# Kernel optimization log

Hardware: AMD Instinct MI355X
Metric: run time of the kernel (lower is better)

The kernel has to match this reference:

```python
import jax, jax.numpy as jnp
import numpy as np

EPS = 1e-6  # LayerNorm eps (added to std, matching torch code)
H = 4       # n_heads
B, D, N, DFF = 8, 512, 1024, 1024


def layer_norm(x, g, b):
    # torch: a_2 * (x - mean) / (std + eps) + b_2, std unbiased (ddof=1)
    m = x.mean(-1, keepdims=True)
    s = x.std(-1, ddof=1, keepdims=True)
    return g * (x - m) / (s + EPS) + b


def mha(q, k, v, W, b):
    # W: [4, d, d] (in->out), b: [4, d]; heads H, d_k = d // H
    Bq, Nq, d = q.shape
    dk = d // H

    def proj(x, i):
        return (x @ W[i] + b[i]).reshape(Bq, -1, H, dk).transpose(0, 2, 1, 3)

    Q, K, V = proj(q, 0), proj(k, 1), proj(v, 2)
    scores = jnp.einsum('bhqd,bhkd->bhqk', Q, K) / np.sqrt(dk).astype(np.float32)
    p = jax.nn.softmax(scores, axis=-1)
    o = jnp.einsum('bhqk,bhkd->bhqd', p, V).transpose(0, 2, 1, 3).reshape(Bq, -1, d)
    return o @ W[3] + b[3]


def ffn(x, w1, b1, w2, b2):
    return jax.nn.relu(x @ w1 + b1) @ w2 + b2


def encoder(x, aw, ab, fw1, fb1, fw2, fb2, lg, lb):
    x = x + mha(layer_norm(x, lg[0], lb[0]), layer_norm(x, lg[0], lb[0]), layer_norm(x, lg[0], lb[0]), aw, ab)
    x = x + ffn(layer_norm(x, lg[1], lb[1]), fw1, fb1, fw2, fb2)
    return layer_norm(x, lg[2], lb[2])


def decoder(x, mem, sw, sb, cw, cb, fw1, fb1, fw2, fb2, lg, lb):
    h0 = layer_norm(x, lg[0], lb[0])
    x = x + mha(h0, h0, h0, sw, sb)
    h1 = layer_norm(x, lg[1], lb[1])
    x = x + mha(h1, mem, mem, cw, cb)
    x = x + ffn(layer_norm(x, lg[2], lb[2]), fw1, fb1, fw2, fb2)
    return layer_norm(x, lg[3], lb[3])


def model(src, tgt, p):
    # src, tgt: [B, N, D]
    mem = encoder(src, p['enc_attn_w'], p['enc_attn_b'], p['enc_ff_w1'], p['enc_ff_b1'],
                  p['enc_ff_w2'], p['enc_ff_b2'], p['enc_ln_g'], p['enc_ln_b'])
    return decoder(tgt, mem, p['dec_sa_w'], p['dec_sa_b'], p['dec_ca_w'], p['dec_ca_b'],
                   p['dec_ff_w1'], p['dec_ff_b1'], p['dec_ff_w2'], p['dec_ff_b2'],
                   p['dec_ln_g'], p['dec_ln_b'])


def setup_inputs() -> dict:
    key = jax.random.key(0)
    ks = jax.random.split(key, 12)
    sc = 0.02
    return {
        'src': jax.random.normal(ks[0], (B, D, N), jnp.float32),
        'tgt': jax.random.normal(ks[1], (B, D, N), jnp.float32),
        'enc_attn_w': jax.random.normal(ks[2], (4, D, D), jnp.float32) * sc,
        'enc_attn_b': jnp.zeros((4, D), jnp.float32),
        'enc_ff_w1': jax.random.normal(ks[3], (D, DFF), jnp.float32) * sc,
        'enc_ff_b1': jnp.zeros((DFF,), jnp.float32),
        'enc_ff_w2': jax.random.normal(ks[4], (DFF, D), jnp.float32) * sc,
        'enc_ff_b2': jnp.zeros((D,), jnp.float32),
        'enc_ln_g': jnp.ones((3, D), jnp.float32),
        'enc_ln_b': jnp.zeros((3, D), jnp.float32),
        'dec_sa_w': jax.random.normal(ks[5], (4, D, D), jnp.float32) * sc,
        'dec_sa_b': jnp.zeros((4, D), jnp.float32),
        'dec_ca_w': jax.random.normal(ks[6], (4, D, D), jnp.float32) * sc,
        'dec_ca_b': jnp.zeros((4, D), jnp.float32),
        'dec_ff_w1': jax.random.normal(ks[7], (D, DFF), jnp.float32) * sc,
        'dec_ff_b1': jnp.zeros((DFF,), jnp.float32),
        'dec_ff_w2': jax.random.normal(ks[8], (DFF, D), jnp.float32) * sc,
        'dec_ff_b2': jnp.zeros((D,), jnp.float32),
        'dec_ln_g': jnp.ones((4, D), jnp.float32),
        'dec_ln_b': jnp.zeros((4, D), jnp.float32),
    }


def reference(src, tgt, enc_attn_w, enc_attn_b, enc_ff_w1, enc_ff_b1, enc_ff_w2, enc_ff_b2,
              enc_ln_g, enc_ln_b, dec_sa_w, dec_sa_b, dec_ca_w, dec_ca_b,
              dec_ff_w1, dec_ff_b1, dec_ff_w2, dec_ff_b2, dec_ln_g, dec_ln_b):
    p = dict(enc_attn_w=enc_attn_w, enc_attn_b=enc_attn_b, enc_ff_w1=enc_ff_w1,
             enc_ff_b1=enc_ff_b1, enc_ff_w2=enc_ff_w2, enc_ff_b2=enc_ff_b2,
             enc_ln_g=enc_ln_g, enc_ln_b=enc_ln_b, dec_sa_w=dec_sa_w, dec_sa_b=dec_sa_b,
             dec_ca_w=dec_ca_w, dec_ca_b=dec_ca_b, dec_ff_w1=dec_ff_w1, dec_ff_b1=dec_ff_b1,
             dec_ff_w2=dec_ff_w2, dec_ff_b2=dec_ff_b2, dec_ln_g=dec_ln_g, dec_ln_b=dec_ln_b)
    s = src.transpose(0, 2, 1)  # [B, N, D]
    t = tgt.transpose(0, 2, 1)
    tgt_embedding = model(s, t, p).transpose(0, 2, 1)  # [B, D, N]
    src_embedding = model(t, s, p).transpose(0, 2, 1)
    return (src_embedding, tgt_embedding)
```

## Files before the change

### kernel.cpp

```cpp
#include <hip/hip_runtime.h>

#define BB 8
#define NN 1024
#define DD 512
#define DFFK 1024
#define HH 4
#define RR (BB * NN)
#define MM (2 * RR)

typedef unsigned short u16;
typedef u16 u16x8 __attribute__((ext_vector_type(8)));
typedef u16 u16x4 __attribute__((ext_vector_type(4)));
typedef float f32x4 __attribute__((ext_vector_type(4)));
typedef __bf16 bf16x8 __attribute__((ext_vector_type(8)));

__device__ __forceinline__ u16 f32_to_bf16(float f) {
  unsigned int u = __builtin_bit_cast(unsigned int, f);
  unsigned int r = u + 0x7FFFu + ((u >> 16) & 1u);
  return (u16)(r >> 16);
}

__device__ __forceinline__ f32x4 mfma16(u16x8 a, u16x8 b, f32x4 c) {
  return __builtin_amdgcn_mfma_f32_16x16x32_bf16(
      __builtin_bit_cast(bf16x8, a), __builtin_bit_cast(bf16x8, b), c, 0, 0, 0);
}

__device__ __forceinline__ void gl16(u16* lds, const u16* g) {
  __builtin_amdgcn_global_load_lds(
      (const __attribute__((address_space(1))) unsigned int*)g,
      (__attribute__((address_space(3))) unsigned int*)lds, 16, 0, 0);
}

__global__ __launch_bounds__(256) void wconv_kernel(const float* __restrict__ W,
                                                    u16* __restrict__ Wt, int K, int N2, int nmat) {
  int idx = blockIdx.x * 256 + threadIdx.x;
  if (idx >= nmat * K * N2) return;
  int mat = idx / (K * N2), rem = idx % (K * N2);
  int k = rem % K, n = rem / K;
  Wt[(size_t)mat * K * N2 + (size_t)n * K + k] =
      f32_to_bf16(W[(size_t)mat * K * N2 + (size_t)k * N2 + n]);
}

__global__ __launch_bounds__(256) void transpose_kernel(const float* __restrict__ in,
                                                        float* __restrict__ out, int R_, int C_) {
  __shared__ float t[32][33];
  int bx = blockIdx.x * 32, by = blockIdx.y * 32;
  size_t zoff = (size_t)blockIdx.z * R_ * C_;
  const float* ip = in + zoff;
  float* op = out + zoff;
  int tx = threadIdx.x, ty = threadIdx.y;
#pragma unroll
  for (int i = 0; i < 32; i += 8)
    t[ty + i][tx] = ip[(size_t)(by + ty + i) * C_ + bx + tx];
  __syncthreads();
#pragma unroll
  for (int i = 0; i < 32; i += 8)
    op[(size_t)(bx + ty + i) * R_ + by + tx] = t[tx][ty + i];
}

__global__ __launch_bounds__(256) void out_trans_kernel(const float* __restrict__ in,
                                                        float* __restrict__ outA,
                                                        float* __restrict__ outB) {
  __shared__ float t[32][33];
  int z = blockIdx.z;
  int dx = blockIdx.x * 32;
  int sy = blockIdx.y * 32;
  int tx = threadIdx.x, ty = threadIdx.y;
  const float* ip = in + (size_t)z * NN * DD;
#pragma unroll
  for (int i = 0; i < 32; i += 8)
    t[ty + i][tx] = ip[(size_t)(sy + ty + i) * DD + dx + tx];
  __syncthreads();
  float* dst = (z < BB) ? (outA + (size_t)z * DD * NN) : (outB + (size_t)(z - BB) * DD * NN);
#pragma unroll
  for (int i = 0; i < 32; i += 8)
    dst[(size_t)(dx + ty + i) * NN + sy + tx] = t[tx][ty + i];
}

__global__ __launch_bounds__(256) void vtrans_kernel(const u16* __restrict__ V, int vstride,
                                                     u16* __restrict__ Vt) {
  __shared__ u16 t[32][33];
  int z = blockIdx.z;
  int b = z >> 2, h = z & 3;
  int sx = blockIdx.x * 32;
  int dy = blockIdx.y * 32;
  int tx = threadIdx.x, ty = threadIdx.y;
  const u16* ip = V + (size_t)b * NN * vstride + h * 128 + dy;
#pragma unroll
  for (int i = 0; i < 32; i += 8)
    t[ty + i][tx] = ip[(size_t)(sx + ty + i) * vstride + tx];
  __syncthreads();
  u16* op = Vt + ((size_t)z * 128 + dy) * NN + sx;
#pragma unroll
  for (int i = 0; i < 32; i += 8)
    op[(size_t)(ty + i) * NN + tx] = t[tx][ty + i];
}

template <int OUTBF>
__global__ __launch_bounds__(256) void ln_kernel(const float* __restrict__ x0,
                                                 const float* __restrict__ x1,
                                                 const float* __restrict__ g,
                                                 const float* __restrict__ bb,
                                                 void* __restrict__ out) {
  int l = threadIdx.x & 63, w = threadIdx.x >> 6;
  size_t row = (size_t)blockIdx.x * 4 + w;
  const float* xr = (row < RR) ? (x0 + row * DD) : (x1 + (row - RR) * DD);
  float4 v0 = *(const float4*)(xr + l * 8);
  float4 v1 = *(const float4*)(xr + l * 8 + 4);
  float sum = v0.x + v0.y + v0.z + v0.w + v1.x + v1.y + v1.z + v1.w;
  float sq = v0.x * v0.x + v0.y * v0.y + v0.z * v0.z + v0.w * v0.w +
             v1.x * v1.x + v1.y * v1.y + v1.z * v1.z + v1.w * v1.w;
#pragma unroll
  for (int o = 1; o < 64; o <<= 1) {
    sum += __shfl_xor(sum, o);
    sq += __shfl_xor(sq, o);
  }
  float mean = sum * (1.0f / DD);
  float var = fmaxf((sq - (float)DD * mean * mean) * (1.0f / (DD - 1)), 0.0f);
  float inv = 1.0f / (sqrtf(var) + 1e-6f);
  float4 g0 = *(const float4*)(g + l * 8), g1 = *(const float4*)(g + l * 8 + 4);
  float4 b0 = *(const float4*)(bb + l * 8), b1 = *(const float4*)(bb + l * 8 + 4);
  float xs[8] = {v0.x, v0.y, v0.z, v0.w, v1.x, v1.y, v1.z, v1.w};
  float gs[8] = {g0.x, g0.y, g0.z, g0.w, g1.x, g1.y, g1.z, g1.w};
  float bs[8] = {b0.x, b0.y, b0.z, b0.w, b1.x, b1.y, b1.z, b1.w};
  float y[8];
#pragma unroll
  for (int j = 0; j < 8; j++) y[j] = (xs[j] - mean) * inv * gs[j] + bs[j];
  if (OUTBF) {
    u16x8 o8;
#pragma unroll
    for (int j = 0; j < 8; j++) o8[j] = f32_to_bf16(y[j]);
    *(u16x8*)((u16*)out + row * DD + l * 8) = o8;
  } else {
    float4 o0 = {y[0], y[1], y[2], y[3]};
    float4 o1 = {y[4], y[5], y[6], y[7]};
    *(float4*)((float*)out + row * DD + l * 8) = o0;
    *(float4*)((float*)out + row * DD + l * 8 + 4) = o1;
  }
}

template <bool RELU, bool OUT_BF16, bool HAS_RES>
__global__ __launch_bounds__(256, 3) void gemm_bt(const u16* __restrict__ A, int lda,
                                                  const u16* __restrict__ Bt,
                                                  const float* __restrict__ bias,
                                                  const float* res0, const float* res1,
                                                  void* Cout, int ldc,
                                                  int N2, int Kd) {
  __shared__ u16 sA[3][512 * 8];
  __shared__ u16 sB[3][512 * 8];
  int tid = threadIdx.x;
  int l = tid & 63, w = tid >> 6;
  int wm = (w >> 1) * 64, wn = (w & 1) * 64;
  int m0 = blockIdx.x * 128, n0 = blockIdx.y * 128;
  f32x4 acc[4][4] = {};

  auto stage = [&](int buf, int k0) {
#pragma unroll
    for (int is = 0; is < 2; is++) {
      int slot = is * 256 + w * 64 + l;
      int chunk = slot >> 7, row = slot & 127;
      gl16(&sA[buf][(size_t)(is * 256 + w * 64) * 8],
           A + (size_t)(m0 + row) * lda + k0 + chunk * 8);
      gl16(&sB[buf][(size_t)(is * 256 + w * 64) * 8],
           Bt + (size_t)(n0 + row) * Kd + k0 + chunk * 8);
    }
  };
  int nt = Kd >> 5;
  stage(0, 0);
  stage(1, 32);
  int bi = 0;
  for (int t = 0; t < nt; t++) {
    if (t + 1 < nt) asm volatile("s_waitcnt vmcnt(4)" ::: "memory");
    else            asm volatile("s_waitcnt vmcnt(0)" ::: "memory");
    __builtin_amdgcn_s_barrier();
    __builtin_amdgcn_sched_barrier(0);
    if (t + 2 < nt) {
      int b2 = bi + 2; if (b2 >= 3) b2 -= 3;
      stage(b2, (t + 2) * 32);
    }
    u16x8 af[4], bf[4];
#pragma unroll
    for (int i = 0; i < 4; i++) {
      af[i] = *(const u16x8*)&sA[bi][((l >> 4) * 128 + wm + i * 16 + (l & 15)) * 8];
      bf[i] = *(const u16x8*)&sB[bi][((l >> 4) * 128 + wn + i * 16 + (l & 15)) * 8];
    }
    __builtin_amdgcn_s_setprio(1);
#pragma unroll
    for (int i = 0; i < 4; i++)
#pragma unroll
      for (int j = 0; j < 4; j++) acc[i][j] = mfma16(af[i], bf[j], acc[i][j]);
    __builtin_amdgcn_s_setprio(0);
    bi = (bi == 2) ? 0 : bi + 1;
  }
  __syncthreads();
  float* eTw = (float*)&sA[0][0] + w * 1024;
  float4 bias4 = *(const float4*)&bias[n0 + wn + (l & 15) * 4];
#pragma unroll
  for (int i = 0; i < 4; i++) {
#pragma unroll
    for (int j = 0; j < 4; j++)
#pragma unroll
      for (int r = 0; r < 4; r++)
        eTw[((l >> 4) * 4 + r) * 64 + j * 16 + (l & 15)] = acc[i][j][r];
#pragma unroll
    for (int t = 0; t < 4; t++) {
      int row = t * 4 + (l >> 4);
      int f4 = l & 15;
      float4 v4 = *(float4*)&eTw[row * 64 + f4 * 4];
      int gm = m0 + wm + i * 16 + row;
      int gn = n0 + wn + f4 * 4;
      v4.x += bias4.x; v4.y += bias4.y; v4.z += bias4.z; v4.w += bias4.w;
      if (RELU) {
        v4.x = fmaxf(v4.x, 0.0f); v4.y = fmaxf(v4.y, 0.0f);
        v4.z = fmaxf(v4.z, 0.0f); v4.w = fmaxf(v4.w, 0.0f);
      }
      if (HAS_RES) {
        const float* rp = (gm < RR) ? (res0 + (size_t)gm * DD)
                                    : (res1 + (size_t)(gm - RR) * DD);
        float4 r4 = *(const float4*)&rp[gn];
        v4.x += r4.x; v4.y += r4.y; v4.z += r4.z; v4.w += r4.w;
      }
      if (OUT_BF16) {
        u16x4 o4;
        o4[0] = f32_to_bf16(v4.x); o4[1] = f32_to_bf16(v4.y);
        o4[2] = f32_to_bf16(v4.z); o4[3] = f32_to_bf16(v4.w);
        *(u16x4*)&((u16*)Cout)[(size_t)gm * ldc + gn] = o4;
      } else {
        *(float4*)&((float*)Cout)[(size_t)gm * ldc + gn] = v4;
      }
    }
  }
}

__global__ __launch_bounds__(512, 4) void attn_kernel(const u16* __restrict__ Q, int qstride,
                                                      const u16* __restrict__ K, int kstride,
                                                      const u16* __restrict__ Vt,
                                                      u16* __restrict__ O, int ostride) {
  __shared__ u16 sK[2][64 * 128];
  __shared__ u16 sV[2][128 * 64];
  __shared__ u16 sP[8][16 * 64];
  int tid = threadIdx.x;
  int l = tid & 63, w = tid >> 6;
  int p = blockIdx.x;
  int xcd = p & 7, slot = p >> 3;
  int qb = slot & 7, ghigh = slot >> 3;
  int g = ghigh * 8 + xcd;
  int b = g >> 2, h = g & 3;
  int q0 = qb * 128 + w * 16;
  int bh = g;

  const u16* Qg = Q + (size_t)b * NN * qstride + h * 128;
  const u16* Kg = K + (size_t)b * NN * kstride + h * 128;
  const u16* Vg = Vt + (size_t)bh * 128 * NN;

  u16x8 qf[4];
#pragma unroll
  for (int c = 0; c < 4; c++)
    qf[c] = *(const u16x8*)(Qg + (size_t)(q0 + (l & 15)) * qstride + c * 32 + (l >> 4) * 8);

  f32x4 oacc[8] = {};
  float psum[4] = {0.0f, 0.0f, 0.0f, 0.0f};
  const float scale = 0.08838834764831843f;

  auto stage = [&](int buf, int k0) {
#pragma unroll
    for (int is = 0; is < 2; is++) {
      int slot2 = is * 512 + tid;
      {
        int row = slot2 >> 4, c16 = slot2 & 15;
        int colb = (c16 * 16) ^ ((row & 7) << 4);
        gl16(&sK[buf][(size_t)(is * 512 + w * 64) * 8],
             Kg + (size_t)(k0 + row) * kstride + (colb >> 1));
      }
      {
        int drow = slot2 >> 3, c16 = slot2 & 7;
        int colb = (c16 * 16) ^ ((drow & 7) << 4);
        gl16(&sV[buf][(size_t)(is * 512 + w * 64) * 8],
             Vg + (size_t)drow * NN + k0 + (colb >> 1));
      }
    }
  };

  stage(0, 0);
  int buf = 0;
  for (int t = 0; t < NN / 64; t++) {
    __syncthreads();
    if (t + 1 < NN / 64) stage(buf ^ 1, (t + 1) * 64);
    f32x4 sc[4] = {};
    __builtin_amdgcn_s_setprio(1);
#pragma unroll
    for (int ks = 0; ks < 4; ks++) {
      int row = ks * 16 + (l & 15);
      int swz = (row & 7) << 4;
#pragma unroll
      for (int c = 0; c < 4; c++) {
        int colb = (c * 64 + (l >> 4) * 16) ^ swz;
        u16x8 kf = *(const u16x8*)&sK[buf][row * 128 + (colb >> 1)];
        sc[ks] = mfma16(qf[c], kf, sc[ks]);
      }
    }
    __builtin_amdgcn_s_setprio(0);
#pragma unroll
    for (int r = 0; r < 4; r++) {
      int prow = (l >> 4) * 4 + r;
      int pswz = (prow & 7) << 4;
#pragma unroll
      for (int ks = 0; ks < 4; ks++) {
        float pp = __expf(sc[ks][r] * scale);
        psum[r] += pp;
        int colb = ((ks * 16 + (l & 15)) * 2) ^ pswz;
        sP[w][prow * 64 + (colb >> 1)] = f32_to_bf16(pp);
      }
    }
    u16x8 pf[2];
#pragma unroll
    for (int kc = 0; kc < 2; kc++) {
      int prow = l & 15;
      int colb = (kc * 64 + (l >> 4) * 16) ^ ((prow & 7) << 4);
      pf[kc] = *(const u16x8*)&sP[w][prow * 64 + (colb >> 1)];
    }
    __builtin_amdgcn_s_setprio(1);
#pragma unroll
    for (int n = 0; n < 8; n++) {
      int drow = n * 16 + (l & 15);
      int swz = (drow & 7) << 4;
#pragma unroll
      for (int kc = 0; kc < 2; kc++) {
        int colb = (kc * 64 + (l >> 4) * 16) ^ swz;
        u16x8 vf = *(const u16x8*)&sV[buf][drow * 64 + (colb >> 1)];
        oacc[n] = mfma16(pf[kc], vf, oacc[n]);
      }
    }
    __builtin_amdgcn_s_setprio(0);
    buf ^= 1;
  }
#pragma unroll
  for (int r = 0; r < 4; r++) {
    psum[r] += __shfl_xor(psum[r], 1);
    psum[r] += __shfl_xor(psum[r], 2);
    psum[r] += __shfl_xor(psum[r], 4);
    psum[r] += __shfl_xor(psum[r], 8);
  }
#pragma unroll
  for (int r = 0; r < 4; r++) {
    float inv = 1.0f / psum[r];
    int grow = q0 + (l >> 4) * 4 + r;
    u16* Op = O + ((size_t)b * NN + grow) * ostride + h * 128 + (l & 15);
#pragma unroll
    for (int n = 0; n < 8; n++) Op[n * 16] = f32_to_bf16(oacc[n][r] * inv);
  }
}

extern "C" void kernel_launch(void* const* d_in, const int* in_sizes, int n_in,
                              void* d_out, int out_size, void* d_ws, size_t ws_size,
                              hipStream_t stream) {
  const float* src = (const float*)d_in[0];
  const float* tgt = (const float*)d_in[1];
  const float* enc_attn_w = (const float*)d_in[2];
  const float* enc_attn_b = (const float*)d_in[3];
  const float* enc_ff_w1 = (const float*)d_in[4];
  const float* enc_ff_b1 = (const float*)d_in[5];
  const float* enc_ff_w2 = (const float*)d_in[6];
  const float* enc_ff_b2 = (const float*)d_in[7];
  const float* enc_ln_g = (const float*)d_in[8];
  const float* enc_ln_b = (const float*)d_in[9];
  const float* dec_sa_w = (const float*)d_in[10];
  const float* dec_sa_b = (const float*)d_in[11];
  const float* dec_ca_w = (const float*)d_in[12];
  const float* dec_ca_b = (const float*)d_in[13];
  const float* dec_ff_w1 = (const float*)d_in[14];
  const float* dec_ff_b1 = (const float*)d_in[15];
  const float* dec_ff_w2 = (const float*)d_in[16];
  const float* dec_ff_b2 = (const float*)d_in[17];
  const float* dec_ln_g = (const float*)d_in[18];
  const float* dec_ln_b = (const float*)d_in[19];

  u16* wp = (u16*)d_ws;
  u16* wE = wp;   wp += 4 * DD * DD;
  u16* wS = wp;   wp += 4 * DD * DD;
  u16* wC = wp;   wp += 4 * DD * DD;
  u16* wEff1 = wp; wp += DD * DFFK;
  u16* wEff2 = wp; wp += DD * DFFK;
  u16* wDff1 = wp; wp += DD * DFFK;
  u16* wDff2 = wp; wp += DD * DFFK;
  char* p = (char*)wp;
  float* sT = (float*)p;  p += (size_t)RR * DD * 4;
  float* tT = (float*)p;  p += (size_t)RR * DD * 4;
  float* xb = (float*)p;  p += (size_t)MM * DD * 4;
  u16* hb = (u16*)p;      p += (size_t)MM * DD * 2;
  u16* memb = (u16*)p;    p += (size_t)MM * DD * 2;
  u16* Vt = (u16*)p;      p += (size_t)16 * HH * 128 * NN * 2;
  u16* U = (u16*)p;       p += (size_t)MM * 3 * DD * 2;
  float* xb1 = xb + (size_t)RR * DD;
  float* xtmp = (float*)U;

  wconv_kernel<<<(4 * DD * DD + 255) / 256, 256, 0, stream>>>(enc_attn_w, wE, DD, DD, 4);
  wconv_kernel<<<(4 * DD * DD + 255) / 256, 256, 0, stream>>>(dec_sa_w, wS, DD, DD, 4);
  wconv_kernel<<<(4 * DD * DD + 255) / 256, 256, 0, stream>>>(dec_ca_w, wC, DD, DD, 4);
  wconv_kernel<<<(DD * DFFK + 255) / 256, 256, 0, stream>>>(enc_ff_w1, wEff1, DD, DFFK, 1);
  wconv_kernel<<<(DD * DFFK + 255) / 256, 256, 0, stream>>>(enc_ff_w2, wEff2, DFFK, DD, 1);
  wconv_kernel<<<(DD * DFFK + 255) / 256, 256, 0, stream>>>(dec_ff_w1, wDff1, DD, DFFK, 1);
  wconv_kernel<<<(DD * DFFK + 255) / 256, 256, 0, stream>>>(dec_ff_w2, wDff2, DFFK, DD, 1);

  transpose_kernel<<<dim3(NN / 32, DD / 32, BB), dim3(32, 8), 0, stream>>>(src, sT, DD, NN);
  transpose_kernel<<<dim3(NN / 32, DD / 32, BB), dim3(32, 8), 0, stream>>>(tgt, tT, DD, NN);

  auto ln = [&](const float* x0, const float* x1, const float* g, const float* b,
                void* out, bool bf) {
    if (bf) ln_kernel<1><<<MM / 4, 256, 0, stream>>>(x0, x1, g, b, out);
    else    ln_kernel<0><<<MM / 4, 256, 0, stream>>>(x0, x1, g, b, out);
  };
  auto gemm = [&](const u16* A, int lda, const u16* W, const float* bias,
                  const float* r0, const float* r1, void* out, int ldc,
                  int N2, int K, int mode) {
    dim3 g(MM / 128, N2 / 128);
    if (mode == 0)
      gemm_bt<false, true, false><<<g, 256, 0, stream>>>(A, lda, W, bias, nullptr, nullptr, out, ldc, N2, K);
    else if (mode == 1)
      gemm_bt<true, true, false><<<g, 256, 0, stream>>>(A, lda, W, bias, nullptr, nullptr, out, ldc, N2, K);
    else
      gemm_bt<false, false, true><<<g, 256, 0, stream>>>(A, lda, W, bias, r0, r1, out, ldc, N2, K);
  };
  auto vtrans = [&]() {
    vtrans_kernel<<<dim3(NN / 32, 4, 64), dim3(32, 8), 0, stream>>>(U + 2 * DD, 3 * DD, Vt);
  };
  auto attn = [&]() {
    attn_kernel<<<dim3(512), 512, 0, stream>>>(U, 3 * DD, U + DD, 3 * DD, Vt,
                                               U + 2 * DD, 3 * DD);
  };
  u16* ab = U + 2 * DD;

  ln(sT, tT, enc_ln_g, enc_ln_b, hb, true);
  gemm(hb, DD, wE, enc_attn_b, nullptr, nullptr, U, 3 * DD, 3 * DD, DD, 0);
  vtrans();
  attn();
  gemm(ab, 3 * DD, wE + 3 * DD * DD, enc_attn_b + 3 * DD, sT, tT, xb, DD, DD, DD, 2);
  ln(xb, xb1, enc_ln_g + DD, enc_ln_b + DD, hb, true);
  gemm(hb, DD, wEff1, enc_ff_b1, nullptr, nullptr, U, DFFK, DFFK, DD, 1);
  gemm(U, DFFK, wEff2, enc_ff_b2, xb, xb1, xb, DD, DD, DFFK, 2);
  ln(xb, xb1, enc_ln_g + 2 * DD, enc_ln_b + 2 * DD, memb, true);
  ln(tT, sT, dec_ln_g, dec_ln_b, hb, true);
  gemm(hb, DD, wS, dec_sa_b, nullptr, nullptr, U, 3 * DD, 3 * DD, DD, 0);
  vtrans();
  attn();
  gemm(ab, 3 * DD, wS + 3 * DD * DD, dec_sa_b + 3 * DD, tT, sT, xb, DD, DD, DD, 2);
  ln(xb, xb1, dec_ln_g + DD, dec_ln_b + DD, hb, true);
  gemm(hb, DD, wC, dec_ca_b, nullptr, nullptr, U, 3 * DD, DD, DD, 0);
  gemm(memb, DD, wC + DD * DD, dec_ca_b + DD, nullptr, nullptr, U + DD, 3 * DD,
       2 * DD, DD, 0);
  vtrans();
  attn();
  gemm(ab, 3 * DD, wC + 3 * DD * DD, dec_ca_b + 3 * DD, xb, xb1, xb, DD, DD, DD, 2);
  ln(xb, xb1, dec_ln_g + 2 * DD, dec_ln_b + 2 * DD, hb, true);
  gemm(hb, DD, wDff1, dec_ff_b1, nullptr, nullptr, U, DFFK, DFFK, DD, 1);
  gemm(U, DFFK, wDff2, dec_ff_b2, xb, xb1, xb, DD, DD, DFFK, 2);
  ln(xb, xb1, dec_ln_g + 3 * DD, dec_ln_b + 3 * DD, xtmp, false);
  float* out_f = (float*)d_out;
  out_trans_kernel<<<dim3(DD / 32, NN / 32, 16), dim3(32, 8), 0, stream>>>(
      xtmp, out_f + (size_t)RR * DD, out_f);
}
```

Measured before the change: 731.9 us.

## Enlarge GEMM tile to 256x128 with 8 waves and BK=64 split-phase pipeline

The bf16 GEMM now uses 512-thread blocks, each computing a 256x128 output tile with a K-step of 64 instead of 32. Each step is split into two halves with a mid-step barrier, so the A and B prefetches for step t+2 are issued separately while MFMAs run. The aim is more reuse per LDS load, fewer barriers per unit of K and better overlap of loads with compute. The cost is larger LDS use (about 144KB with triple buffering), fewer resident blocks and a grid with half as many blocks along M.

```diff
diff --git a/kernel.cpp b/kernel.cpp
--- a/kernel.cpp
+++ b/kernel.cpp
@@ -140,57 +140,88 @@
 }
 
 template <bool RELU, bool OUT_BF16, bool HAS_RES>
-__global__ __launch_bounds__(256, 3) void gemm_bt(const u16* __restrict__ A, int lda,
+__global__ __launch_bounds__(512, 2) void gemm_bt(const u16* __restrict__ A, int lda,
                                                   const u16* __restrict__ Bt,
                                                   const float* __restrict__ bias,
                                                   const float* res0, const float* res1,
                                                   void* Cout, int ldc,
                                                   int N2, int Kd) {
-  __shared__ u16 sA[3][512 * 8];
-  __shared__ u16 sB[3][512 * 8];
+  __shared__ u16 sA[3][2048 * 8];
+  __shared__ u16 sB[3][1024 * 8];
   int tid = threadIdx.x;
   int l = tid & 63, w = tid >> 6;
   int wm = (w >> 1) * 64, wn = (w & 1) * 64;
-  int m0 = blockIdx.x * 128, n0 = blockIdx.y * 128;
+  int m0 = blockIdx.x * 256, n0 = blockIdx.y * 128;
   f32x4 acc[4][4] = {};
 
-  auto stage = [&](int buf, int k0) {
+  auto stageA = [&](int buf, int k0) {
+#pragma unroll
+    for (int is = 0; is < 4; is++) {
+      int slot = is * 512 + tid;
+      int chunk = slot >> 8, row = slot & 255;
+      gl16(&sA[buf][(size_t)(is * 512 + w * 64) * 8],
+           A + (size_t)(m0 + row) * lda + k0 + chunk * 8);
+    }
+  };
+  auto stageB = [&](int buf, int k0) {
 #pragma unroll
     for (int is = 0; is < 2; is++) {
-      int slot = is * 256 + w * 64 + l;
+      int slot = is * 512 + tid;
       int chunk = slot >> 7, row = slot & 127;
-      gl16(&sA[buf][(size_t)(is * 256 + w * 64) * 8],
-           A + (size_t)(m0 + row) * lda + k0 + chunk * 8);
-      gl16(&sB[buf][(size_t)(is * 256 + w * 64) * 8],
+      gl16(&sB[buf][(size_t)(is * 512 + w * 64) * 8],
            Bt + (size_t)(n0 + row) * Kd + k0 + chunk * 8);
     }
   };
-  int nt = Kd >> 5;
-  stage(0, 0);
-  stage(1, 32);
+  int NT = Kd >> 6;
+  stageA(0, 0); stageB(0, 0);
+  stageA(1, 64); stageB(1, 64);
   int bi = 0;
-  for (int t = 0; t < nt; t++) {
-    if (t + 1 < nt) asm volatile("s_waitcnt vmcnt(4)" ::: "memory");
+  for (int t = 0; t < NT; t++) {
+    if (t + 1 < NT) asm volatile("s_waitcnt vmcnt(6)" ::: "memory");
     else            asm volatile("s_waitcnt vmcnt(0)" ::: "memory");
     __builtin_amdgcn_s_barrier();
     __builtin_amdgcn_sched_barrier(0);
-    if (t + 2 < nt) {
-      int b2 = bi + 2; if (b2 >= 3) b2 -= 3;
-      stage(b2, (t + 2) * 32);
-    }
-    u16x8 af[4], bf[4];
-#pragma unroll
-    for (int i = 0; i < 4; i++) {
-      af[i] = *(const u16x8*)&sA[bi][((l >> 4) * 128 + wm + i * 16 + (l & 15)) * 8];
-      bf[i] = *(const u16x8*)&sB[bi][((l >> 4) * 128 + wn + i * 16 + (l & 15)) * 8];
-    }
+    int b2 = bi + 2; if (b2 >= 3) b2 -= 3;
+    int k2 = (t + 2) * 64;
+    u16x8 bfr[4][2], afr[2][2];
+#pragma unroll
+    for (int j = 0; j < 4; j++)
+#pragma unroll
+      for (int ks = 0; ks < 2; ks++)
+        bfr[j][ks] = *(const u16x8*)&sB[bi][((size_t)(ks * 4 + (l >> 4)) * 128 + wn + j * 16 + (l & 15)) * 8];
+#pragma unroll
+    for (int i = 0; i < 2; i++)
+#pragma unroll
+      for (int ks = 0; ks < 2; ks++)
+        afr[i][ks] = *(const u16x8*)&sA[bi][((size_t)(ks * 4 + (l >> 4)) * 256 + wm + i * 16 + (l & 15)) * 8];
+    if (t + 2 < NT) stageA(b2, k2);
     __builtin_amdgcn_s_setprio(1);
 #pragma unroll
-    for (int i = 0; i < 4; i++)
-#pragma unroll
-      for (int j = 0; j < 4; j++) acc[i][j] = mfma16(af[i], bf[j], acc[i][j]);
+    for (int ks = 0; ks < 2; ks++)
+#pragma unroll
+      for (int i = 0; i < 2; i++)
+#pragma unroll
+        for (int j = 0; j < 4; j++)
+          acc[i][j] = mfma16(afr[i][ks], bfr[j][ks], acc[i][j]);
     __builtin_amdgcn_s_setprio(0);
-    bi = (bi == 2) ? 0 : bi + 1;
+    __builtin_amdgcn_s_barrier();
+    u16x8 afr2[2][2];
+#pragma unroll
+    for (int i = 0; i < 2; i++)
+#pragma unroll
+      for (int ks = 0; ks < 2; ks++)
+        afr2[i][ks] = *(const u16x8*)&sA[bi][((size_t)(ks * 4 + (l >> 4)) * 256 + wm + (i + 2) * 16 + (l & 15)) * 8];
+    if (t + 2 < NT) stageB(b2, k2);
+    __builtin_amdgcn_s_setprio(1);
+#pragma unroll
+    for (int ks = 0; ks < 2; ks++)
+#pragma unroll
+      for (int i = 0; i < 2; i++)
+#pragma unroll
+        for (int j = 0; j < 4; j++)
+          acc[i + 2][j] = mfma16(afr2[i][ks], bfr[j][ks], acc[i + 2][j]);
+    __builtin_amdgcn_s_setprio(0);
+    bi++; if (bi >= 3) bi = 0;
   }
   __syncthreads();
   float* eTw = (float*)&sA[0][0] + w * 1024;
@@ -413,13 +444,13 @@
   auto gemm = [&](const u16* A, int lda, const u16* W, const float* bias,
                   const float* r0, const float* r1, void* out, int ldc,
                   int N2, int K, int mode) {
-    dim3 g(MM / 128, N2 / 128);
+    dim3 g(MM / 256, N2 / 128);
     if (mode == 0)
-      gemm_bt<false, true, false><<<g, 256, 0, stream>>>(A, lda, W, bias, nullptr, nullptr, out, ldc, N2, K);
+      gemm_bt<false, true, false><<<g, 512, 0, stream>>>(A, lda, W, bias, nullptr, nullptr, out, ldc, N2, K);
     else if (mode == 1)
-      gemm_bt<true, true, false><<<g, 256, 0, stream>>>(A, lda, W, bias, nullptr, nullptr, out, ldc, N2, K);
+      gemm_bt<true, true, false><<<g, 512, 0, stream>>>(A, lda, W, bias, nullptr, nullptr, out, ldc, N2, K);
     else
-      gemm_bt<false, false, true><<<g, 256, 0, stream>>>(A, lda, W, bias, r0, r1, out, ldc, N2, K);
+      gemm_bt<false, false, true><<<g, 512, 0, stream>>>(A, lda, W, bias, r0, r1, out, ldc, N2, K);
   };
   auto vtrans = [&]() {
     vtrans_kernel<<<dim3(NN / 32, 4, 64), dim3(32, 8), 0, stream>>>(U + 2 * DD, 3 * DD, Vt);
```

Result: faster. 673.4 us (-8.0%).
